# Optimization experiments

Hardware: AMD Instinct MI355X
Metric: run time of the kernel (lower is better)

The kernel has to match this reference:

```python
import jax, jax.numpy as jnp
import numpy as np

NUM_USERS = 100000
NUM_ITEMS = 50000
N_NODES = NUM_USERS + NUM_ITEMS
NUM_COMMUNITY = 64
N_LAYERS = 3
NNZ = 2400000
BATCH = 8192
NEG_SLOPE = 0.1
EPS = 1e-12


def setup_inputs() -> dict:
    key = jax.random.key(0)
    ks = jax.random.split(key, 9)
    stdv = 1.0 / np.sqrt(NUM_COMMUNITY)
    return {
        "users": jax.random.randint(ks[0], (BATCH,), 0, NUM_USERS, dtype=jnp.int64 if jax.config.jax_enable_x64 else jnp.int32).astype(jnp.int32),
        "adjacent_items": jax.random.randint(ks[1], (BATCH,), 0, NUM_ITEMS).astype(jnp.int32),
        "weak_items": jax.random.randint(ks[2], (BATCH,), 0, NUM_ITEMS).astype(jnp.int32),
        "strong_items": jax.random.randint(ks[3], (BATCH,), 0, NUM_ITEMS).astype(jnp.int32),
        "edge_rows": jax.random.randint(ks[4], (NNZ,), 0, N_NODES).astype(jnp.int32),
        "edge_cols": jax.random.randint(ks[5], (NNZ,), 0, N_NODES).astype(jnp.int32),
        "edge_vals": jax.random.uniform(ks[6], (NNZ,), dtype=jnp.float32),
        "user_preference": jax.random.uniform(ks[7], (NUM_USERS, NUM_COMMUNITY), dtype=jnp.float32, minval=-stdv, maxval=stdv),
        "item_preference": jax.random.uniform(ks[8], (NUM_ITEMS, NUM_COMMUNITY), dtype=jnp.float32, minval=-stdv, maxval=stdv),
    }


def _lrelu_l2norm(x):
    # leaky_relu(neg_slope=0.1) then L2-normalize along last dim (torch F.normalize semantics)
    x = jnp.where(x >= 0, x, NEG_SLOPE * x)
    norm = jnp.sqrt(jnp.sum(x * x, axis=-1, keepdims=True))
    return x / jnp.maximum(norm, EPS)


def reference(users, adjacent_items, weak_items, strong_items,
              edge_rows, edge_cols, edge_vals,
              user_preference, item_preference):
    # ---- computer(): LightGCN-style propagation over sparse adjacency ----
    pref = _lrelu_l2norm(jnp.concatenate([user_preference, item_preference], axis=0))  # [N, C]
    acc = pref
    p = pref
    for _ in range(N_LAYERS):
        # sparse.mm(Graph, p): gather source rows, scale by edge values, scatter-add into dest rows
        msg = edge_vals[:, None] * p[edge_cols]                      # [nnz, C]
        p = jax.ops.segment_sum(msg, edge_rows, num_segments=N_NODES)  # [N, C]
        p = _lrelu_l2norm(p)
        acc = acc + p
    merged = acc / (N_LAYERS + 1)  # mean over stacked layers
    users_pref = merged[:NUM_USERS]
    items_pref = merged[NUM_USERS:]

    # ---- forward(): per-pair dot products + sigmoid ----
    u = users_pref[users]  # [B, C]

    def score(items):
        return jax.nn.sigmoid(jnp.sum(u * items_pref[items], axis=-1))

    # stack of (adjacent, weak, strong) gamma preferences, shape [3, B]
    return jnp.stack([score(adjacent_items), score(weak_items), score(strong_items)], axis=0)
```

## Files before the change

kernel.cpp:

```cpp
#include <hip/hip_runtime.h>
#include <math.h>

#define D 64
#define NUM_USERS 100000
#define NUM_ITEMS 50000
#define N_NODES 150000
#define NNZ 2400000
#define BATCH 8192
#define NEG_SLOPE 0.1f
#define EPS_NRM 1e-12f

#define NBUCKET 586
#define NCHUNK  256
#define CH      9375
#define NH      (NBUCKET * NCHUNK)
#define NBH     (NH / 256)
#define CAP     6144
#define VSCALE  16383.f

typedef unsigned short ushort_t;

__device__ __forceinline__ float wave_sum64(float v) {
    #pragma unroll
    for (int off = 32; off > 0; off >>= 1)
        v += __shfl_xor(v, off, 64);
    return v;
}

__device__ __forceinline__ int wave_sum64_i(int v) {
    #pragma unroll
    for (int off = 32; off > 0; off >>= 1)
        v += __shfl_xor(v, off, 64);
    return v;
}

__device__ __forceinline__ float bf2f(ushort_t u) {
    return __uint_as_float(((unsigned)u) << 16);
}
__device__ __forceinline__ ushort_t f2bf(float f) {
    unsigned x = __float_as_uint(f);
    unsigned r = (x + 0x7FFFu + ((x >> 16) & 1u)) >> 16;
    return (ushort_t)r;
}


__global__ void bucket_hist(const int* __restrict__ rows, int* __restrict__ ht) {
    __shared__ int hist[NBUCKET];
    int c = blockIdx.x, tid = threadIdx.x;
    for (int b = tid; b < NBUCKET; b += 256) hist[b] = 0;
    __syncthreads();
    int base = c * CH;
    for (int i = tid; i < CH; i += 256)
        atomicAdd(&hist[rows[base + i] >> 8], 1);
    __syncthreads();
    for (int b = tid; b < NBUCKET; b += 256) ht[b * NCHUNK + c] = hist[b];
}

__global__ void scan1_kernel(const int* __restrict__ in, int* __restrict__ out,
                             int* __restrict__ bsums, int n) {
    int tid = threadIdx.x, gid = blockIdx.x * 256 + tid;
    int v = (gid < n) ? in[gid] : 0;
    int lane = tid & 63, w = tid >> 6;
    int s = v;
    #pragma unroll
    for (int off = 1; off < 64; off <<= 1) {
        int t = __shfl_up(s, off, 64);
        if (lane >= off) s += t;
    }
    __shared__ int wsum[4];
    if (lane == 63) wsum[w] = s;
    __syncthreads();
    if (tid == 0) {
        int a = 0;
        #pragma unroll
        for (int i = 0; i < 4; i++) { int t = wsum[i]; wsum[i] = a; a += t; }
    }
    __syncthreads();
    int incl = s + wsum[w];
    if (gid < n) out[gid] = incl - v;
    if (tid == 255) bsums[blockIdx.x] = incl;
}

__global__ void scan3_kernel(int* __restrict__ out, const int* __restrict__ bsums, int n) {
    __shared__ int wtot[4];
    __shared__ int total;
    int b = blockIdx.x, tid = threadIdx.x;
    int lane = tid & 63, w = tid >> 6;
    int partial = 0;
    for (int i = tid; i < b; i += 256) partial += bsums[i];
    partial = wave_sum64_i(partial);
    if (lane == 0) wtot[w] = partial;
    __syncthreads();
    if (tid == 0) total = wtot[0] + wtot[1] + wtot[2] + wtot[3];
    __syncthreads();
    int gid = b * 256 + tid;
    if (gid < n) out[gid] += total;
}

__global__ void __launch_bounds__(512) bucket_scatter(
        const int* __restrict__ rows, const int* __restrict__ cols,
        const float* __restrict__ vals, const int* __restrict__ hoff,
        int2* __restrict__ est) {
    __shared__ int cur[NBUCKET];
    int c = blockIdx.x, tid = threadIdx.x;
    for (int b = tid; b < NBUCKET; b += 512) cur[b] = hoff[b * NCHUNK + c];
    __syncthreads();
    int base = c * CH;
    for (int i = tid; i < CH; i += 512) {
        int e = base + i;
        int r = rows[e];
        int pos = atomicAdd(&cur[r >> 8], 1);
        est[pos] = make_int2(cols[e] | ((r & 255) << 18), __float_as_int(vals[e]));
    }
}

__global__ void __launch_bounds__(1024) bucket_sort(const int2* __restrict__ est,
                                                    const int* __restrict__ hoff,
                                                    unsigned* __restrict__ es,
                                                    int* __restrict__ rowptr) {
    __shared__ int      hist[256];
    __shared__ int      wsum[4];
    __shared__ unsigned outbuf[CAP];
    int b = blockIdx.x, tid = threadIdx.x;
    int beg = hoff[b * NCHUNK];
    int end = (b == NBUCKET - 1) ? NNZ : hoff[(b + 1) * NCHUNK];
    if (tid < 256) hist[tid] = 0;
    __syncthreads();
    for (int i = beg + tid; i < end; i += 1024)
        atomicAdd(&hist[est[i].x >> 18], 1);
    __syncthreads();
    int excl = 0;
    if (tid < 256) {
        int v = hist[tid];
        int lane = tid & 63, w = tid >> 6;
        int s = v;
        #pragma unroll
        for (int off = 1; off < 64; off <<= 1) {
            int t = __shfl_up(s, off, 64);
            if (lane >= off) s += t;
        }
        if (lane == 63) wsum[w] = s;
        excl = s - v;
    }
    __syncthreads();
    if (tid == 0) {
        int a = 0;
        #pragma unroll
        for (int i = 0; i < 4; i++) { int t = wsum[i]; wsum[i] = a; a += t; }
    }
    __syncthreads();
    if (tid < 256) {
        excl += wsum[tid >> 6];
        int r = (b << 8) + tid;
        if (r <= N_NODES) rowptr[r] = beg + excl;
        hist[tid] = excl;
    }
    __syncthreads();
    for (int i = beg + tid; i < end; i += 1024) {
        int2 kv = est[i];
        int d = atomicAdd(&hist[kv.x >> 18], 1);
        float val = __int_as_float(kv.y);
        unsigned vq = (unsigned)(val * VSCALE + 0.5f);
        outbuf[d] = ((unsigned)kv.x & 0x3FFFFu) | (vq << 18);
    }
    __syncthreads();
    int n = end - beg;
    for (int i = tid; i < n; i += 1024)
        es[beg + i] = outbuf[i];
}

__global__ void init_kernel(const float* __restrict__ upref,
                            const float* __restrict__ ipref,
                            ushort_t* __restrict__ p0) {
    int row  = blockIdx.x * 4 + (threadIdx.x >> 6);
    int lane = threadIdx.x & 63;
    if (row >= N_NODES) return;
    float x = (row < NUM_USERS) ? upref[(size_t)row * D + lane]
                                : ipref[(size_t)(row - NUM_USERS) * D + lane];
    x = (x >= 0.f) ? x : NEG_SLOPE * x;
    float norm = sqrtf(wave_sum64(x * x));
    float y = x / fmaxf(norm, EPS_NRM);
    p0[(size_t)row * D + lane] = f2bf(y);
}

__global__ void gather_kernel(const int* __restrict__ rowptr,
                              const unsigned* __restrict__ es,
                              const ushort_t* __restrict__ p,
                              ushort_t* __restrict__ pn) {
    int row  = blockIdx.x * 4 + (threadIdx.x >> 6);
    int lane = threadIdx.x & 63;
    if (row >= N_NODES) return;
    int sub = lane >> 3;
    int fl  = lane & 7;
    int beg = rowptr[row], end = rowptr[row + 1];

    float a[8];
    #pragma unroll
    for (int k = 0; k < 8; k++) a[k] = 0.f;

    const float vs = 1.f / VSCALE;
    int e = beg + sub;
    while (e + 8 < end) {
        unsigned ev0 = es[e];
        unsigned ev1 = es[e + 8];
        const uint4 q0 = *(const uint4*)(p + (((ev0 & 0x3FFFFu) << 6) | (fl << 3)));
        const uint4 q1 = *(const uint4*)(p + (((ev1 & 0x3FFFFu) << 6) | (fl << 3)));
        float v0 = (float)(ev0 >> 18) * vs;
        float v1 = (float)(ev1 >> 18) * vs;
        a[0] = fmaf(v0, __uint_as_float(q0.x << 16),         a[0]);
        a[1] = fmaf(v0, __uint_as_float(q0.x & 0xFFFF0000u), a[1]);
        a[2] = fmaf(v0, __uint_as_float(q0.y << 16),         a[2]);
        a[3] = fmaf(v0, __uint_as_float(q0.y & 0xFFFF0000u), a[3]);
        a[4] = fmaf(v0, __uint_as_float(q0.z << 16),         a[4]);
        a[5] = fmaf(v0, __uint_as_float(q0.z & 0xFFFF0000u), a[5]);
        a[6] = fmaf(v0, __uint_as_float(q0.w << 16),         a[6]);
        a[7] = fmaf(v0, __uint_as_float(q0.w & 0xFFFF0000u), a[7]);
        a[0] = fmaf(v1, __uint_as_float(q1.x << 16),         a[0]);
        a[1] = fmaf(v1, __uint_as_float(q1.x & 0xFFFF0000u), a[1]);
        a[2] = fmaf(v1, __uint_as_float(q1.y << 16),         a[2]);
        a[3] = fmaf(v1, __uint_as_float(q1.y & 0xFFFF0000u), a[3]);
        a[4] = fmaf(v1, __uint_as_float(q1.z << 16),         a[4]);
        a[5] = fmaf(v1, __uint_as_float(q1.z & 0xFFFF0000u), a[5]);
        a[6] = fmaf(v1, __uint_as_float(q1.w << 16),         a[6]);
        a[7] = fmaf(v1, __uint_as_float(q1.w & 0xFFFF0000u), a[7]);
        e += 16;
    }
    if (e < end) {
        unsigned ev = es[e];
        const uint4 q = *(const uint4*)(p + (((ev & 0x3FFFFu) << 6) | (fl << 3)));
        float v = (float)(ev >> 18) * vs;
        a[0] = fmaf(v, __uint_as_float(q.x << 16),         a[0]);
        a[1] = fmaf(v, __uint_as_float(q.x & 0xFFFF0000u), a[1]);
        a[2] = fmaf(v, __uint_as_float(q.y << 16),         a[2]);
        a[3] = fmaf(v, __uint_as_float(q.y & 0xFFFF0000u), a[3]);
        a[4] = fmaf(v, __uint_as_float(q.z << 16),         a[4]);
        a[5] = fmaf(v, __uint_as_float(q.z & 0xFFFF0000u), a[5]);
        a[6] = fmaf(v, __uint_as_float(q.w << 16),         a[6]);
        a[7] = fmaf(v, __uint_as_float(q.w & 0xFFFF0000u), a[7]);
    }

    bool s0 = (sub & 1) != 0, s1 = (sub & 2) != 0, s2 = (sub & 4) != 0;
    float b[4];
    #pragma unroll
    for (int j = 0; j < 4; j++) {
        float send = s0 ? a[2 * j]     : a[2 * j + 1];
        float keep = s0 ? a[2 * j + 1] : a[2 * j];
        b[j] = keep + __shfl_xor(send, 8, 64);
    }
    float c[2];
    #pragma unroll
    for (int i = 0; i < 2; i++) {
        float send = s1 ? b[2 * i]     : b[2 * i + 1];
        float keep = s1 ? b[2 * i + 1] : b[2 * i];
        c[i] = keep + __shfl_xor(send, 16, 64);
    }
    float y;
    {
        float send = s2 ? c[0] : c[1];
        float keep = s2 ? c[1] : c[0];
        y = keep + __shfl_xor(send, 32, 64);
    }

    y = (y >= 0.f) ? y : NEG_SLOPE * y;
    float ss = wave_sum64(y * y);
    float inv = 1.f / fmaxf(sqrtf(ss), EPS_NRM);
    pn[(size_t)row * D + fl * 8 + sub] = f2bf(y * inv);
}

__global__ void score_kernel(const int* __restrict__ users,
                             const int* __restrict__ it0,
                             const int* __restrict__ it1,
                             const int* __restrict__ it2,
                             const ushort_t* __restrict__ p0,
                             const ushort_t* __restrict__ p1,
                             const ushort_t* __restrict__ p2,
                             const ushort_t* __restrict__ p3,
                             float* __restrict__ out) {
    int b    = blockIdx.x * 4 + (threadIdx.x >> 6);
    int lane = threadIdx.x & 63;
    if (b >= BATCH) return;
    int u = users[b];
    size_t uo = (size_t)u * D + lane;
    float uf = bf2f(p0[uo]) + bf2f(p1[uo]) + bf2f(p2[uo]) + bf2f(p3[uo]);

    int its[3];
    its[0] = it0[b]; its[1] = it1[b]; its[2] = it2[b];
    #pragma unroll
    for (int k = 0; k < 3; k++) {
        size_t io = (size_t)(NUM_USERS + its[k]) * D + lane;
        float itf = bf2f(p0[io]) + bf2f(p1[io]) + bf2f(p2[io]) + bf2f(p3[io]);
        float s = wave_sum64(uf * itf) * 0.0625f;
        if (lane == 0)
            out[k * BATCH + b] = 1.f / (1.f + expf(-s));
    }
}

extern "C" void kernel_launch(void* const* d_in, const int* in_sizes, int n_in,
                              void* d_out, int out_size, void* d_ws, size_t ws_size,
                              hipStream_t stream) {
    const int*   users  = (const int*)  d_in[0];
    const int*   adj    = (const int*)  d_in[1];
    const int*   weak   = (const int*)  d_in[2];
    const int*   strong = (const int*)  d_in[3];
    const int*   erows  = (const int*)  d_in[4];
    const int*   ecols  = (const int*)  d_in[5];
    const float* evals  = (const float*)d_in[6];
    const float* upref  = (const float*)d_in[7];
    const float* ipref  = (const float*)d_in[8];
    float* out = (float*)d_out;

    const size_t rowElems = (size_t)N_NODES * D;

    char* base = (char*)d_ws;
    size_t off = 0;
    auto alloc = [&](size_t bytes) {
        char* p = base + off;
        off = (off + bytes + 255) & ~(size_t)255;
        return (void*)p;
    };
    ushort_t* p0     = (ushort_t*)alloc(rowElems * sizeof(ushort_t));
    ushort_t* p1     = (ushort_t*)alloc(rowElems * sizeof(ushort_t));
    ushort_t* p2     = (ushort_t*)alloc(rowElems * sizeof(ushort_t));
    ushort_t* p3     = (ushort_t*)alloc(rowElems * sizeof(ushort_t));
    unsigned* es     = (unsigned*)alloc((size_t)NNZ * sizeof(unsigned));
    int*      ht     = (int*)     alloc((size_t)NH * sizeof(int));
    int*      hoff   = (int*)     alloc((size_t)NH * sizeof(int));
    int*      rowptr = (int*)     alloc((N_NODES + 1) * sizeof(int));
    int*      bsums  = (int*)     alloc(1024 * sizeof(int));
    int2*     est    = (int2*)p2;

    bucket_hist   <<<NCHUNK, 256, 0, stream>>>(erows, ht);
    scan1_kernel  <<<NBH, 256, 0, stream>>>(ht, hoff, bsums, NH);
    scan3_kernel  <<<NBH, 256, 0, stream>>>(hoff, bsums, NH);
    bucket_scatter<<<NCHUNK, 512, 0, stream>>>(erows, ecols, evals, hoff, est);
    bucket_sort   <<<NBUCKET, 1024, 0, stream>>>(est, hoff, es, rowptr);

    init_kernel<<<(N_NODES + 3) / 4, 256, 0, stream>>>(upref, ipref, p0);
    gather_kernel<<<(N_NODES + 3) / 4, 256, 0, stream>>>(rowptr, es, p0, p1);
    gather_kernel<<<(N_NODES + 3) / 4, 256, 0, stream>>>(rowptr, es, p1, p2);
    gather_kernel<<<(N_NODES + 3) / 4, 256, 0, stream>>>(rowptr, es, p2, p3);

    score_kernel<<<(BATCH + 3) / 4, 256, 0, stream>>>(users, adj, weak, strong,
                                                      p0, p1, p2, p3, out);
}
```

Baseline: 378.4 us.

## Replace two-level bucket sort CSR build with global atomic histogram and scatter

Replaces the bucketed, chunked histogram plus in-shared-memory local sort with a direct per-row global atomic histogram, a scan over 150016 rows, and a global-atomic scatter into CSR. This removes the intermediate int2 staging array and the bucket_sort pass, cutting passes over the edge list. In exchange it relies on contended global atomics and random global writes, and edge order within each row becomes nondeterministic, which changes floating-point summation order.

```diff
diff --git a/kernel.cpp b/kernel.cpp
--- a/kernel.cpp
+++ b/kernel.cpp
@@ -10,12 +10,8 @@
 #define NEG_SLOPE 0.1f
 #define EPS_NRM 1e-12f
 
-#define NBUCKET 586
-#define NCHUNK  256
-#define CH      9375
-#define NH      (NBUCKET * NCHUNK)
+#define NH      150016
 #define NBH     (NH / 256)
-#define CAP     6144
 #define VSCALE  16383.f
 
 typedef unsigned short ushort_t;
@@ -44,16 +40,17 @@
 }
 
 
-__global__ void bucket_hist(const int* __restrict__ rows, int* __restrict__ ht) {
-    __shared__ int hist[NBUCKET];
-    int c = blockIdx.x, tid = threadIdx.x;
-    for (int b = tid; b < NBUCKET; b += 256) hist[b] = 0;
-    __syncthreads();
-    int base = c * CH;
-    for (int i = tid; i < CH; i += 256)
-        atomicAdd(&hist[rows[base + i] >> 8], 1);
-    __syncthreads();
-    for (int b = tid; b < NBUCKET; b += 256) ht[b * NCHUNK + c] = hist[b];
+__global__ void row_hist(const int* __restrict__ rows, int* __restrict__ hist) {
+    int i = blockIdx.x * 256 + threadIdx.x;
+    int stride = gridDim.x * 256;
+    const int4* r4 = (const int4*)rows;
+    for (; i < NNZ / 4; i += stride) {
+        int4 r = r4[i];
+        atomicAdd(&hist[r.x], 1);
+        atomicAdd(&hist[r.y], 1);
+        atomicAdd(&hist[r.z], 1);
+        atomicAdd(&hist[r.w], 1);
+    }
 }
 
 __global__ void scan1_kernel(const int* __restrict__ in, int* __restrict__ out,
@@ -81,7 +78,8 @@
     if (tid == 255) bsums[blockIdx.x] = incl;
 }
 
-__global__ void scan3_kernel(int* __restrict__ out, const int* __restrict__ bsums, int n) {
+__global__ void scan3_kernel(int* __restrict__ out, int* __restrict__ cursor,
+                             const int* __restrict__ bsums, int n) {
     __shared__ int wtot[4];
     __shared__ int total;
     int b = blockIdx.x, tid = threadIdx.x;
@@ -94,79 +92,34 @@
     if (tid == 0) total = wtot[0] + wtot[1] + wtot[2] + wtot[3];
     __syncthreads();
     int gid = b * 256 + tid;
-    if (gid < n) out[gid] += total;
-}
-
-__global__ void __launch_bounds__(512) bucket_scatter(
-        const int* __restrict__ rows, const int* __restrict__ cols,
-        const float* __restrict__ vals, const int* __restrict__ hoff,
-        int2* __restrict__ est) {
-    __shared__ int cur[NBUCKET];
-    int c = blockIdx.x, tid = threadIdx.x;
-    for (int b = tid; b < NBUCKET; b += 512) cur[b] = hoff[b * NCHUNK + c];
-    __syncthreads();
-    int base = c * CH;
-    for (int i = tid; i < CH; i += 512) {
-        int e = base + i;
-        int r = rows[e];
-        int pos = atomicAdd(&cur[r >> 8], 1);
-        est[pos] = make_int2(cols[e] | ((r & 255) << 18), __float_as_int(vals[e]));
-    }
-}
-
-__global__ void __launch_bounds__(1024) bucket_sort(const int2* __restrict__ est,
-                                                    const int* __restrict__ hoff,
-                                                    unsigned* __restrict__ es,
-                                                    int* __restrict__ rowptr) {
-    __shared__ int      hist[256];
-    __shared__ int      wsum[4];
-    __shared__ unsigned outbuf[CAP];
-    int b = blockIdx.x, tid = threadIdx.x;
-    int beg = hoff[b * NCHUNK];
-    int end = (b == NBUCKET - 1) ? NNZ : hoff[(b + 1) * NCHUNK];
-    if (tid < 256) hist[tid] = 0;
-    __syncthreads();
-    for (int i = beg + tid; i < end; i += 1024)
-        atomicAdd(&hist[est[i].x >> 18], 1);
-    __syncthreads();
-    int excl = 0;
-    if (tid < 256) {
-        int v = hist[tid];
-        int lane = tid & 63, w = tid >> 6;
-        int s = v;
-        #pragma unroll
-        for (int off = 1; off < 64; off <<= 1) {
-            int t = __shfl_up(s, off, 64);
-            if (lane >= off) s += t;
-        }
-        if (lane == 63) wsum[w] = s;
-        excl = s - v;
-    }
-    __syncthreads();
-    if (tid == 0) {
-        int a = 0;
-        #pragma unroll
-        for (int i = 0; i < 4; i++) { int t = wsum[i]; wsum[i] = a; a += t; }
-    }
-    __syncthreads();
-    if (tid < 256) {
-        excl += wsum[tid >> 6];
-        int r = (b << 8) + tid;
-        if (r <= N_NODES) rowptr[r] = beg + excl;
-        hist[tid] = excl;
-    }
-    __syncthreads();
-    for (int i = beg + tid; i < end; i += 1024) {
-        int2 kv = est[i];
-        int d = atomicAdd(&hist[kv.x >> 18], 1);
-        float val = __int_as_float(kv.y);
-        unsigned vq = (unsigned)(val * VSCALE + 0.5f);
-        outbuf[d] = ((unsigned)kv.x & 0x3FFFFu) | (vq << 18);
-    }
-    __syncthreads();
-    int n = end - beg;
-    for (int i = tid; i < n; i += 1024)
-        es[beg + i] = outbuf[i];
+    if (gid < n) {
+        int v = out[gid] + total;
+        out[gid] = v;
+        cursor[gid] = v;
+    }
+}
+
+__global__ void csr_scatter(const int* __restrict__ rows, const int* __restrict__ cols,
+                            const float* __restrict__ vals, int* __restrict__ cursor,
+                            unsigned* __restrict__ es) {
+    int i = blockIdx.x * 256 + threadIdx.x;
+    int stride = gridDim.x * 256;
+    const int4*   r4 = (const int4*)rows;
+    const int4*   c4 = (const int4*)cols;
+    const float4* v4 = (const float4*)vals;
+    for (; i < NNZ / 4; i += stride) {
+        int4 r = r4[i];
+        int4 c = c4[i];
+        float4 v = v4[i];
+        int p0 = atomicAdd(&cursor[r.x], 1);
+        es[p0] = (unsigned)c.x | ((unsigned)(v.x * VSCALE + 0.5f) << 18);
+        int p1 = atomicAdd(&cursor[r.y], 1);
+        es[p1] = (unsigned)c.y | ((unsigned)(v.y * VSCALE + 0.5f) << 18);
+        int p2 = atomicAdd(&cursor[r.z], 1);
+        es[p2] = (unsigned)c.z | ((unsigned)(v.z * VSCALE + 0.5f) << 18);
+        int p3 = atomicAdd(&cursor[r.w], 1);
+        es[p3] = (unsigned)c.w | ((unsigned)(v.w * VSCALE + 0.5f) << 18);
+    }
 }
 
 __global__ void init_kernel(const float* __restrict__ upref,
@@ -323,17 +276,16 @@
     ushort_t* p2     = (ushort_t*)alloc(rowElems * sizeof(ushort_t));
     ushort_t* p3     = (ushort_t*)alloc(rowElems * sizeof(ushort_t));
     unsigned* es     = (unsigned*)alloc((size_t)NNZ * sizeof(unsigned));
-    int*      ht     = (int*)     alloc((size_t)NH * sizeof(int));
-    int*      hoff   = (int*)     alloc((size_t)NH * sizeof(int));
-    int*      rowptr = (int*)     alloc((N_NODES + 1) * sizeof(int));
+    int*      hist   = (int*)     alloc((size_t)NH * sizeof(int));
+    int*      rowptr = (int*)     alloc((size_t)NH * sizeof(int));
+    int*      cursor = (int*)     alloc((size_t)NH * sizeof(int));
     int*      bsums  = (int*)     alloc(1024 * sizeof(int));
-    int2*     est    = (int2*)p2;
-
-    bucket_hist   <<<NCHUNK, 256, 0, stream>>>(erows, ht);
-    scan1_kernel  <<<NBH, 256, 0, stream>>>(ht, hoff, bsums, NH);
-    scan3_kernel  <<<NBH, 256, 0, stream>>>(hoff, bsums, NH);
-    bucket_scatter<<<NCHUNK, 512, 0, stream>>>(erows, ecols, evals, hoff, est);
-    bucket_sort   <<<NBUCKET, 1024, 0, stream>>>(est, hoff, es, rowptr);
+
+    hipMemsetAsync(hist, 0, (size_t)NH * sizeof(int), stream);
+    row_hist   <<<2048, 256, 0, stream>>>(erows, hist);
+    scan1_kernel<<<NBH, 256, 0, stream>>>(hist, rowptr, bsums, NH);
+    scan3_kernel<<<NBH, 256, 0, stream>>>(rowptr, cursor, bsums, NH);
+    csr_scatter<<<2048, 256, 0, stream>>>(erows, ecols, evals, cursor, es);
 
     init_kernel<<<(N_NODES + 3) / 4, 256, 0, stream>>>(upref, ipref, p0);
     gather_kernel<<<(N_NODES + 3) / 4, 256, 0, stream>>>(rowptr, es, p0, p1);
```

New measurement: 553.3 us. 1.46x slower.
